# Performance work log

Measured on AMD Instinct MI355X. Metric: run time of the kernel, lower is better.

## Reference

```python
import jax, jax.numpy as jnp
import numpy as np

EPS = 1e-6
SKIP_THR = 0.35     # AdaptiveComputeBlock skip_threshold
ENERGY_THR = 0.95   # AdaptiveRankLinear energy_threshold


def rms_norm(x, w):
    return x * jax.lax.rsqrt(jnp.mean(x * x, axis=-1, keepdims=True) + EPS) * w


def ternary_quantize(w):
    # absmean quantization: round(w/scale) clamped to {-1,0,+1}, rescaled
    s = jnp.maximum(jnp.mean(jnp.abs(w)), 1e-8)
    return jnp.clip(jnp.round(w / s), -1.0, 1.0) * s


def setup_inputs() -> dict:
    key = jax.random.key(0)
    ks = jax.random.split(key, 16)
    D, H, depth, R, N = 2048, 8192, 2, 16, 4096
    inp = {
        "x": jax.random.normal(ks[0], (N, D), jnp.float32),
        "acb_norm_w": jnp.ones((depth, D), jnp.float32),
        "router_w": jax.random.normal(ks[1], (depth, D), jnp.float32) * 0.02,
        "w1": jax.random.normal(ks[2], (depth, H, D), jnp.float32) * 0.02,
        "w2": jax.random.normal(ks[3], (depth, D, H), jnp.float32) * 0.02,
        "w3": jax.random.normal(ks[4], (depth, H, D), jnp.float32) * 0.02,
        "acb_gamma": jax.random.uniform(ks[5], (depth, D), jnp.float32) * 1e-2,
        "arl_norm_w": jnp.ones((depth, D), jnp.float32),
        "U": jax.random.normal(ks[6], (depth, D, R), jnp.float32) * 0.02,
        "S": jax.random.normal(ks[7], (depth, R), jnp.float32),
        "V": jax.random.normal(ks[8], (depth, R, D), jnp.float32) * 0.02,
        "arl_gamma": jax.random.uniform(ks[9], (depth, D), jnp.float32) * 1e-2,
        "bit_norm_w": jnp.ones((depth, D), jnp.float32),
        "w_up": jax.random.normal(ks[10], (depth, H, D), jnp.float32) * 0.02,
        "w_down": jax.random.normal(ks[11], (depth, D, H), jnp.float32) * 0.02,
        "bit_gamma": jax.random.uniform(ks[12], (depth, D), jnp.float32) * 1e-2,
    }
    return inp


def reference(x, acb_norm_w, router_w, w1, w2, w3, acb_gamma,
              arl_norm_w, U, S, V, arl_gamma,
              bit_norm_w, w_up, w_down, bit_gamma):
    depth = acb_norm_w.shape[0]
    for d in range(depth):
        # ---- AdaptiveComputeBlock (eval path: hard router mask, no gate scaling)
        xn = rms_norm(x, acb_norm_w[d])                    # [N, D]
        gates = jax.nn.sigmoid(xn @ router_w[d])           # [N]
        active = (gates > SKIP_THR)[..., None]             # [N, 1]
        h = jax.nn.silu(xn @ w1[d].T) * (xn @ w3[d].T)     # [N, H] SwiGLU
        ffn = h @ w2[d].T                                  # [N, D]
        x = x + jnp.where(active, ffn * acb_gamma[d], 0.0)

        # ---- AdaptiveRankLinear (effective-rank mask from singular energy)
        xn = rms_norm(x, arl_norm_w[d])
        s_abs = jnp.abs(S[d])
        cum = jnp.cumsum(s_abs) / jnp.maximum(jnp.sum(s_abs), 1e-8)
        # index i kept iff i < r, r = first index with cum >= threshold (plus 1)
        keep = jnp.concatenate([jnp.ones((1,), bool), cum[:-1] < ENERGY_THR])
        low = (xn @ U[d]) * (S[d] * keep)                  # [N, R]
        x = x + (low @ V[d]) * arl_gamma[d]

        # ---- BitLinear (eval path: ternary weights, fp activations)
        xn = rms_norm(x, bit_norm_w[d])
        hq = jax.nn.silu(xn @ ternary_quantize(w_up[d]).T)  # [N, H]
        x = x + (hq @ ternary_quantize(w_down[d]).T) * bit_gamma[d]
    return x
```

## Files before the change

### kernel.cpp

```cpp
#include <hip/hip_runtime.h>

#define D_DIM 2048
#define H_DIM 8192
#define NTOK  4096
#define R_DIM 16
#define DEPTH 2

typedef float f32x4 __attribute__((ext_vector_type(4)));
typedef unsigned short u16x4 __attribute__((ext_vector_type(4)));
typedef unsigned short u16x8 __attribute__((ext_vector_type(8)));
typedef int i32x2 __attribute__((ext_vector_type(2)));
typedef int i32x4 __attribute__((ext_vector_type(4)));

typedef __attribute__((address_space(1))) void void_g;
typedef __attribute__((address_space(3))) void void_l;

__device__ __forceinline__ unsigned short f2bf(float f){
  __bf16 b = (__bf16)f;
  return __builtin_bit_cast(unsigned short, b);
}
__device__ __forceinline__ float bf2f(unsigned short u){
  unsigned int x = ((unsigned int)u) << 16;
  return __builtin_bit_cast(float, x);
}

__device__ __forceinline__ float wredf(float v){
#pragma unroll
  for(int o=32;o;o>>=1) v += __shfl_xor(v,o,64);
  return v;
}
__device__ __forceinline__ float wredmax(float v){
#pragma unroll
  for(int o=32;o;o>>=1) v = fmaxf(v, __shfl_xor(v,o,64));
  return v;
}
__device__ __forceinline__ double wredd(double v){
#pragma unroll
  for(int o=32;o;o>>=1) v += __shfl_xor(v,o,64);
  return v;
}

__device__ __forceinline__ void gload_lds16(const void* g, void* l){
  __builtin_amdgcn_global_load_lds((void_g*)g, (void_l*)l, 16, 0, 0);
}

__device__ __forceinline__ int clampi(int v, int lim){
  return v > lim ? lim : (v < -lim ? -lim : v);
}
__device__ __forceinline__ int pack4q(float a, float b, float c, float d,
                                      float inv, int lim){
  int qa = clampi((int)rintf(a*inv), lim);
  int qb = clampi((int)rintf(b*inv), lim);
  int qc = clampi((int)rintf(c*inv), lim);
  int qd = clampi((int)rintf(d*inv), lim);
  return (qa&255) | ((qb&255)<<8) | ((qc&255)<<16) | ((qd&255)<<24);
}

__global__ __launch_bounds__(256) void rowpass1_i8(
    const float* __restrict__ x, const float* __restrict__ nw,
    const float* __restrict__ rw, signed char* __restrict__ xq,
    float* __restrict__ sxn, float* __restrict__ act)
{
  const int row = blockIdx.x, tid = threadIdx.x;
  const int lane = tid & 63, wid = tid >> 6;
  const float* xr = x + (size_t)row*D_DIM + tid*8;
  f32x4 v0 = *(const f32x4*)xr;
  f32x4 v1 = *(const f32x4*)(xr+4);
  float ssq = 0.0f;
#pragma unroll
  for(int j=0;j<4;++j) ssq += v0[j]*v0[j] + v1[j]*v1[j];
  __shared__ float red[4];
  float t = wredf(ssq);
  if(lane==0) red[wid] = t;
  __syncthreads();
  const float rs = rsqrtf((red[0]+red[1]+red[2]+red[3])*(1.0f/D_DIM) + 1e-6f);

  f32x4 n0 = *(const f32x4*)(nw + tid*8);
  f32x4 n1 = *(const f32x4*)(nw + tid*8 + 4);
  f32x4 r0 = *(const f32x4*)(rw + tid*8);
  f32x4 r1 = *(const f32x4*)(rw + tid*8 + 4);
  float a[8];
  float gp = 0.0f, am = 0.0f;
#pragma unroll
  for(int j=0;j<4;++j){
    a[j]   = v0[j]*rs*n0[j];
    a[4+j] = v1[j]*rs*n1[j];
    gp += a[j]*r0[j] + a[4+j]*r1[j];
    am = fmaxf(am, fmaxf(fabsf(a[j]), fabsf(a[4+j])));
  }
  float wm = wredmax(am);
  __syncthreads();
  if(lane==0) red[wid] = wm;
  __syncthreads();
  const float rowmax = fmaxf(fmaxf(red[0],red[1]), fmaxf(red[2],red[3]));
  const float guard = fmaxf(rowmax, 1e-12f);
  const float inv = 127.0f/guard;
  i32x2 q;
  q[0] = pack4q(a[0],a[1],a[2],a[3], inv, 127);
  q[1] = pack4q(a[4],a[5],a[6],a[7], inv, 127);
  *(i32x2*)(xq + (size_t)row*D_DIM + tid*8) = q;

  float gd = wredf(gp);
  __syncthreads();
  if(lane==0) red[wid] = gd;
  __syncthreads();
  if(tid==0){
    sxn[row] = guard/127.0f;
    float dot = red[0]+red[1]+red[2]+red[3];
    float g = 1.0f/(1.0f+expf(-dot));
    act[row] = (g > 0.35f) ? 1.0f : 0.0f;
  }
}

__global__ __launch_bounds__(256) void buildmap(const float* __restrict__ act,
                                                int* __restrict__ rowmap,
                                                int* __restrict__ cntp)
{
  const int tid = threadIdx.x;
  const int lane = tid & 63, wid = tid >> 6;
  int flags[16]; int c = 0;
#pragma unroll
  for(int j=0;j<16;++j){
    flags[j] = (act[tid*16+j] != 0.0f) ? 1 : 0;
    c += flags[j];
  }
  int inc = c;
#pragma unroll
  for(int o=1;o<64;o<<=1){
    int t = __shfl_up(inc, o, 64);
    if(lane >= o) inc += t;
  }
  __shared__ int wsum[4];
  if(lane==63) wsum[wid] = inc;
  __syncthreads();
  int base = inc - c;
  for(int w=0;w<wid;++w) base += wsum[w];
  const int total = wsum[0]+wsum[1]+wsum[2]+wsum[3];
#pragma unroll
  for(int j=0;j<16;++j){
    if(flags[j]) rowmap[base++] = tid*16+j;
  }
  if(tid==0) cntp[0] = total;
  __syncthreads();
  for(int i = total + tid; i < NTOK; i += 256) rowmap[i] = 0;
}

__global__ __launch_bounds__(256) void rowpass2_i8(
    float* __restrict__ x, const float* __restrict__ anw,
    const float* __restrict__ U, const float* __restrict__ Sv,
    const float* __restrict__ V, const float* __restrict__ agam,
    const float* __restrict__ bnw, signed char* __restrict__ xq,
    float* __restrict__ sxn)
{
  const int row = blockIdx.x, tid = threadIdx.x;
  const int lane = tid & 63, wid = tid >> 6;
  float* xr = x + (size_t)row*D_DIM + tid*8;
  f32x4 v0 = *(const f32x4*)xr;
  f32x4 v1 = *(const f32x4*)(xr+4);
  float ssq = 0.0f;
#pragma unroll
  for(int j=0;j<4;++j) ssq += v0[j]*v0[j] + v1[j]*v1[j];
  __shared__ float red[4];
  float t = wredf(ssq);
  if(lane==0) red[wid] = t;
  __syncthreads();
  const float rs = rsqrtf((red[0]+red[1]+red[2]+red[3])*(1.0f/D_DIM) + 1e-6f);

  f32x4 a0 = *(const f32x4*)(anw + tid*8);
  f32x4 a1 = *(const f32x4*)(anw + tid*8 + 4);
  float xn2[8];
#pragma unroll
  for(int j=0;j<4;++j){ xn2[j] = v0[j]*rs*a0[j]; xn2[4+j] = v1[j]*rs*a1[j]; }

  float pl[16];
#pragma unroll
  for(int r2=0;r2<16;++r2) pl[r2] = 0.0f;
#pragma unroll
  for(int j=0;j<8;++j){
    const int k = tid*8 + j;
    const f32x4* Up = (const f32x4*)(U + (size_t)k*R_DIM);
    f32x4 u0=Up[0], u1=Up[1], u2=Up[2], u3=Up[3];
    const float xv = xn2[j];
#pragma unroll
    for(int q=0;q<4;++q){
      pl[q]    += xv*u0[q];
      pl[4+q]  += xv*u1[q];
      pl[8+q]  += xv*u2[q];
      pl[12+q] += xv*u3[q];
    }
  }
#pragma unroll
  for(int r2=0;r2<16;++r2) pl[r2] = wredf(pl[r2]);
  __shared__ float lred[4][16];
  if(lane==0){
#pragma unroll
    for(int r2=0;r2<16;++r2) lred[wid][r2] = pl[r2];
  }
  __syncthreads();
  __shared__ float lowS[16];
  if(tid==0){
    float sa[16]; float totS = 0.0f;
#pragma unroll
    for(int r2=0;r2<16;++r2){ sa[r2] = fabsf(Sv[r2]); totS += sa[r2]; }
    totS = fmaxf(totS, 1e-8f);
    float c = 0.0f;
#pragma unroll
    for(int r2=0;r2<16;++r2){
      float lraw = lred[0][r2]+lred[1][r2]+lred[2][r2]+lred[3][r2];
      float keep = (r2==0) ? 1.0f : ((c/totS < 0.95f) ? 1.0f : 0.0f);
      c += sa[r2];
      lowS[r2] = lraw * Sv[r2] * keep;
    }
  }
  __syncthreads();

  f32x4 d0 = {0,0,0,0}, d1 = {0,0,0,0};
#pragma unroll
  for(int r2=0;r2<16;++r2){
    const float lr = lowS[r2];
    const f32x4* Vp = (const f32x4*)(V + (size_t)r2*D_DIM + tid*8);
    f32x4 q0 = Vp[0], q1 = Vp[1];
#pragma unroll
    for(int j=0;j<4;++j){ d0[j] += lr*q0[j]; d1[j] += lr*q1[j]; }
  }
  f32x4 g0 = *(const f32x4*)(agam + tid*8);
  f32x4 g1 = *(const f32x4*)(agam + tid*8 + 4);
  f32x4 xo0, xo1;
  float ssq2 = 0.0f;
#pragma unroll
  for(int j=0;j<4;++j){
    xo0[j] = v0[j] + d0[j]*g0[j];
    xo1[j] = v1[j] + d1[j]*g1[j];
    ssq2 += xo0[j]*xo0[j] + xo1[j]*xo1[j];
  }
  __syncthreads();
  float t2 = wredf(ssq2);
  if(lane==0) red[wid] = t2;
  __syncthreads();
  const float rs2 = rsqrtf((red[0]+red[1]+red[2]+red[3])*(1.0f/D_DIM) + 1e-6f);
  f32x4 b0 = *(const f32x4*)(bnw + tid*8);
  f32x4 b1 = *(const f32x4*)(bnw + tid*8 + 4);
  float a[8]; float am = 0.0f;
#pragma unroll
  for(int j=0;j<4;++j){
    a[j]   = xo0[j]*rs2*b0[j];
    a[4+j] = xo1[j]*rs2*b1[j];
    am = fmaxf(am, fmaxf(fabsf(a[j]), fabsf(a[4+j])));
  }
  *(f32x4*)xr = xo0;
  *(f32x4*)(xr+4) = xo1;

  float wm = wredmax(am);
  __syncthreads();
  if(lane==0) red[wid] = wm;
  __syncthreads();
  const float rowmax = fmaxf(fmaxf(red[0],red[1]), fmaxf(red[2],red[3]));
  const float guard = fmaxf(rowmax, 1e-12f);
  const float inv = 127.0f/guard;
  i32x2 q;
  q[0] = pack4q(a[0],a[1],a[2],a[3], inv, 127);
  q[1] = pack4q(a[4],a[5],a[6],a[7], inv, 127);
  *(i32x2*)(xq + (size_t)row*D_DIM + tid*8) = q;
  if(tid==0) sxn[row] = guard/127.0f;
}

__global__ __launch_bounds__(256) void hquant(
    const unsigned short* __restrict__ h, signed char* __restrict__ q,
    float* __restrict__ sh, const int* __restrict__ cntp)
{
  const int row = blockIdx.x, tid = threadIdx.x;
  if(cntp && row >= cntp[0]) return;
  const int lane = tid & 63, wid = tid >> 6;
  const unsigned short* hr = h + (size_t)row*H_DIM + tid*32;
  float v[32]; float am = 0.0f;
#pragma unroll
  for(int c=0;c<4;++c){
    u16x8 u = *(const u16x8*)(hr + c*8);
#pragma unroll
    for(int j=0;j<8;++j){
      float f = bf2f(u[j]);
      v[c*8+j] = f;
      am = fmaxf(am, fabsf(f));
    }
  }
  __shared__ float red[4];
  float wm = wredmax(am);
  if(lane==0) red[wid] = wm;
  __syncthreads();
  const float rowmax = fmaxf(fmaxf(red[0],red[1]), fmaxf(red[2],red[3]));
  const float guard = fmaxf(rowmax, 1e-12f);
  const float inv = 127.0f/guard;
  i32x4 o0, o1;
#pragma unroll
  for(int c=0;c<4;++c)
    o0[c] = pack4q(v[c*4],v[c*4+1],v[c*4+2],v[c*4+3], inv, 127);
#pragma unroll
  for(int c=0;c<4;++c)
    o1[c] = pack4q(v[16+c*4],v[16+c*4+1],v[16+c*4+2],v[16+c*4+3], inv, 127);
  signed char* qp = q + (size_t)row*H_DIM + tid*32;
  *(i32x4*)qp = o0;
  *(i32x4*)(qp+16) = o1;
  if(tid==0) sh[row] = guard/127.0f;
}

template<int C>
__global__ __launch_bounds__(256) void wquant_row(const float* __restrict__ w,
                                                  signed char* __restrict__ q,
                                                  float* __restrict__ srow)
{
  constexpr int PER = C/256;
  const int row = blockIdx.x, tid = threadIdx.x;
  const int lane = tid & 63, wid = tid >> 6;
  const float* wr = w + (size_t)row*C + tid*PER;
  float v[PER];
  float am = 0.0f;
#pragma unroll
  for(int j=0;j<PER;j+=4){
    f32x4 t = *(const f32x4*)(wr+j);
#pragma unroll
    for(int e=0;e<4;++e){ v[j+e] = t[e]; am = fmaxf(am, fabsf(t[e])); }
  }
  float wm = wredmax(am);
  __shared__ float red[4];
  if(lane==0) red[wid] = wm;
  __syncthreads();
  const float guard = fmaxf(fmaxf(fmaxf(red[0],red[1]),fmaxf(red[2],red[3])),
                            1e-12f);
  const float inv = 127.0f/guard;
  signed char* qr = q + (size_t)row*C + tid*PER;
#pragma unroll
  for(int j=0;j<PER;j+=8){
    i32x2 o;
    o[0] = pack4q(v[j],v[j+1],v[j+2],v[j+3], inv, 127);
    o[1] = pack4q(v[j+4],v[j+5],v[j+6],v[j+7], inv, 127);
    *(i32x2*)(qr+j) = o;
  }
  if(tid==0) srow[row] = guard/127.0f;
}

__global__ __launch_bounds__(256) void wq2(
    const float* __restrict__ wa, const float* __restrict__ wb,
    signed char* __restrict__ qa, signed char* __restrict__ qb,
    float* __restrict__ sa, float* __restrict__ sb)
{
  const int bid = blockIdx.x, tid = threadIdx.x;
  const int lane = tid & 63, wid = tid >> 6;
  const int row = (bid < H_DIM) ? bid : bid - H_DIM;
  const float* src = ((bid < H_DIM) ? wa : wb) + (size_t)row*D_DIM + tid*8;
  signed char* dq  = ((bid < H_DIM) ? qa : qb) + (size_t)row*D_DIM + tid*8;
  float* sd        = ((bid < H_DIM) ? sa : sb) + row;
  f32x4 v0 = *(const f32x4*)src;
  f32x4 v1 = *(const f32x4*)(src+4);
  float am = 0.0f;
#pragma unroll
  for(int e=0;e<4;++e)
    am = fmaxf(am, fmaxf(fabsf(v0[e]), fabsf(v1[e])));
  float wm = wredmax(am);
  __shared__ float red[4];
  if(lane==0) red[wid] = wm;
  __syncthreads();
  const float guard = fmaxf(fmaxf(fmaxf(red[0],red[1]),fmaxf(red[2],red[3])),
                            1e-12f);
  const float inv = 127.0f/guard;
  i32x2 o;
  o[0] = pack4q(v0[0],v0[1],v0[2],v0[3], inv, 127);
  o[1] = pack4q(v1[0],v1[1],v1[2],v1[3], inv, 127);
  *(i32x2*)dq = o;
  if(tid==0) *sd = guard/127.0f;
}

__global__ __launch_bounds__(256) void abs_part2(const float* __restrict__ wa,
                                                 const float* __restrict__ wb,
                                                 double* __restrict__ part)
{
  const long long n4 = (long long)H_DIM*D_DIM/4;
  const int bid = blockIdx.x, tid = threadIdx.x;
  const int lane = tid & 63, wid = tid >> 6;
  const float* w = (bid < 1024) ? wa : wb;
  const int sub = bid & 1023;
  float s = 0.0f;
  for(long long i = (long long)sub*256 + tid; i < n4; i += 1024*256){
    f32x4 v = ((const f32x4*)w)[i];
    s += fabsf(v[0]) + fabsf(v[1]) + fabsf(v[2]) + fabsf(v[3]);
  }
  double ds = wredd((double)s);
  __shared__ double sred[4];
  if(lane==0) sred[wid] = ds;
  __syncthreads();
  if(tid==0) part[bid] = sred[0]+sred[1]+sred[2]+sred[3];
}

__global__ __launch_bounds__(256) void abs_final2(const double* __restrict__ part,
                                                  float* __restrict__ scale)
{
  const int tid = threadIdx.x;
  const int lane = tid & 63, wid = tid >> 6;
  double s0 = 0.0, s1 = 0.0;
  for(int i=tid;i<1024;i+=256){ s0 += part[i]; s1 += part[1024+i]; }
  s0 = wredd(s0); s1 = wredd(s1);
  __shared__ double sred[2][4];
  if(lane==0){ sred[0][wid] = s0; sred[1][wid] = s1; }
  __syncthreads();
  if(tid==0){
    double m0 = (sred[0][0]+sred[0][1]+sred[0][2]+sred[0][3])
                / ((double)H_DIM*(double)D_DIM);
    double m1 = (sred[1][0]+sred[1][1]+sred[1][2]+sred[1][3])
                / ((double)H_DIM*(double)D_DIM);
    scale[0] = (float)fmax(m0, 1e-8);
    scale[1] = (float)fmax(m1, 1e-8);
  }
}

__global__ __launch_bounds__(256) void tquant2(const float* __restrict__ wa,
                                               const float* __restrict__ wb,
                                               const float* __restrict__ scale,
                                               signed char* __restrict__ qa,
                                               signed char* __restrict__ qb)
{
  const long long n8 = (long long)H_DIM*D_DIM/8;
  const int bid = blockIdx.x;
  const bool first = (bid < 2048);
  const float* w = first ? wa : wb;
  signed char* q = first ? qa : qb;
  const float inv = 1.0f/scale[first ? 0 : 1];
  const int sub = first ? bid : bid - 2048;
  for(long long i = (long long)sub*256 + threadIdx.x; i < n8; i += 2048*256){
    f32x4 a = ((const f32x4*)w)[2*i];
    f32x4 b = ((const f32x4*)w)[2*i+1];
    i32x2 o;
    o[0] = pack4q(a[0],a[1],a[2],a[3], inv, 1);
    o[1] = pack4q(b[0],b[1],b[2],b[3], inv, 1);
    ((i32x2*)q)[i] = o;
  }
}

template<int EPI>
__global__ __launch_bounds__(256, 2) void gemmq(
    const signed char* __restrict__ A,
    const signed char* __restrict__ B0,
    const signed char* __restrict__ B1,
    const int Nout, const int K,
    const float* __restrict__ sArow,
    const float* __restrict__ sW0,
    const float* __restrict__ sW1,
    const int* __restrict__ rowmap,
    const int* __restrict__ cntp,
    unsigned short* __restrict__ obf,
    float* __restrict__ xacc,
    const float* __restrict__ gamma)
{
  constexpr bool DUAL    = (EPI==0);
  constexpr bool GATHER  = (EPI==0);
  constexpr bool SCATTER = (EPI==2);
  constexpr bool CMP     = GATHER || SCATTER;

  __shared__ __align__(16) signed char smA[128*128];
  __shared__ __align__(16) signed char smB[128*128];
  __shared__ __align__(16) signed char smB2[DUAL?(128*128):16];

  int cnt = 0;
  if constexpr (CMP) cnt = cntp[0];
  const int padded = CMP ? ((cnt+127)&~127) : (1<<30);

  const int tid  = threadIdx.x;
  const int lane = tid & 63;
  const int wid  = tid >> 6;
  const int wr   = wid >> 1;
  const int wc   = wid & 1;
  const int frow = lane & 15;
  const int k16  = lane >> 4;

  const int nwg = (int)gridDim.x;
  const int bid = (int)blockIdx.x;
  const int swz = ((bid & 7) * (nwg >> 3)) + (bid >> 3);
  const int rowBase = (swz & 31) << 7;
  const int colBase = (swz >> 5) << 7;

  if constexpr (CMP){ if(rowBase >= padded) return; }

  const signed char* Asrc[4];
  const signed char* Bsrc[4];
  const signed char* B2src[4];
#pragma unroll
  for(int u=0;u<4;++u){
    int L = u*256 + tid;
    int row = L >> 3, c = L & 7;
    int soff = (c ^ (row & 7)) * 16;
    int arow;
    if constexpr (GATHER) arow = rowmap[rowBase + row];
    else                  arow = rowBase + row;
    Asrc[u] = A + (size_t)arow*K + soff;
    Bsrc[u] = B0 + (size_t)(colBase + row)*K + soff;
    if constexpr (DUAL) B2src[u] = B1 + (size_t)(colBase + row)*K + soff;
  }

  const i32x4 izero = {0,0,0,0};
  i32x4 acc[4][4];
  i32x4 acc2[4][4];
#pragma unroll
  for(int m=0;m<4;++m)
#pragma unroll
    for(int n=0;n<4;++n){ acc[m][n] = izero; acc2[m][n] = izero; }

  for(int k0=0;k0<K;k0+=128){
#pragma unroll
    for(int u=0;u<4;++u) gload_lds16(Asrc[u]+k0, &smA[u*4096 + tid*16]);
#pragma unroll
    for(int u=0;u<4;++u) gload_lds16(Bsrc[u]+k0, &smB[u*4096 + tid*16]);
    if constexpr (DUAL){
#pragma unroll
      for(int u=0;u<4;++u) gload_lds16(B2src[u]+k0, &smB2[u*4096 + tid*16]);
    }
    __syncthreads();

#pragma unroll
    for(int ks=0;ks<2;++ks){
      i32x4 af[4], bfr[4], bfr2[4];
#pragma unroll
      for(int m=0;m<4;++m){
        int rr = (wr<<6)+(m<<4)+frow;
        int cc = (ks*4 + k16) ^ (rr & 7);
        af[m] = *(const i32x4*)&smA[rr*128 + cc*16];
      }
#pragma unroll
      for(int n=0;n<4;++n){
        int rr = (wc<<6)+(n<<4)+frow;
        int cc = (ks*4 + k16) ^ (rr & 7);
        bfr[n] = *(const i32x4*)&smB[rr*128 + cc*16];
        if constexpr (DUAL) bfr2[n] = *(const i32x4*)&smB2[rr*128 + cc*16];
      }
#pragma unroll
      for(int m=0;m<4;++m)
#pragma unroll
        for(int n=0;n<4;++n){
          acc[m][n] = __builtin_amdgcn_mfma_i32_16x16x64_i8(af[m], bfr[n], acc[m][n], 0,0,0);
          if constexpr (DUAL)
            acc2[m][n] = __builtin_amdgcn_mfma_i32_16x16x64_i8(af[m], bfr2[n], acc2[m][n], 0,0,0);
        }
    }
    __syncthreads();
  }

  float fsW0 = 0.0f;
  if constexpr (EPI==1 || EPI==3) fsW0 = sW0[0];
  const int growB = rowBase + (wr<<6) + (k16<<2);
  const int gcolB = colBase + (wc<<6) + frow;
#pragma unroll
  for(int m=0;m<4;++m){
#pragma unroll
    for(int n=0;n<4;++n){
      const int grow0 = growB + (m<<4);
      const int gcol  = gcolB + (n<<4);
      i32x4 v = acc[m][n];
      if constexpr (EPI==0){
        i32x4 v2 = acc2[m][n];
        const float w0 = sW0[gcol];
        const float w1s = sW1[gcol];
#pragma unroll
        for(int j=0;j<4;++j){
          const int mc = grow0 + j;
          const float sa = sArow[rowmap[mc]];
          float f1 = (float)v[j]  * sa * w0;
          float f3 = (float)v2[j] * sa * w1s;
          float hv = (f1/(1.0f+__expf(-f1))) * f3;
          obf[(size_t)mc*Nout + gcol] = f2bf(hv);
        }
      } else if constexpr (EPI==1){
#pragma unroll
        for(int j=0;j<4;++j){
          const int mc = grow0 + j;
          const float sa = sArow[mc];
          float f = (float)v[j] * sa * fsW0;
          obf[(size_t)mc*Nout + gcol] = f2bf(f/(1.0f+__expf(-f)));
        }
      } else if constexpr (EPI==2){
        const float gw = sW0[gcol]*gamma[gcol];
#pragma unroll
        for(int j=0;j<4;++j){
          const int mc = grow0 + j;
          if(mc < cnt){
            const float sa = sArow[mc];
            xacc[(size_t)rowmap[mc]*Nout + gcol] += (float)v[j] * sa * gw;
          }
        }
      } else {
        const float gw = fsW0*gamma[gcol];
#pragma unroll
        for(int j=0;j<4;++j){
          const int mc = grow0 + j;
          const float sa = sArow[mc];
          xacc[(size_t)mc*Nout + gcol] += (float)v[j] * sa * gw;
        }
      }
    }
  }
}

extern "C" void kernel_launch(void* const* d_in, const int* in_sizes, int n_in,
                              void* d_out, int out_size, void* d_ws, size_t ws_size,
                              hipStream_t stream)
{
  (void)in_sizes; (void)n_in; (void)out_size; (void)ws_size;
  const float* x_in  = (const float*)d_in[0];
  const float* acbnw = (const float*)d_in[1];
  const float* routw = (const float*)d_in[2];
  const float* w1    = (const float*)d_in[3];
  const float* w2    = (const float*)d_in[4];
  const float* w3    = (const float*)d_in[5];
  const float* acbg  = (const float*)d_in[6];
  const float* arlnw = (const float*)d_in[7];
  const float* U     = (const float*)d_in[8];
  const float* Sv    = (const float*)d_in[9];
  const float* V     = (const float*)d_in[10];
  const float* arlg  = (const float*)d_in[11];
  const float* bitnw = (const float*)d_in[12];
  const float* wup   = (const float*)d_in[13];
  const float* wdn   = (const float*)d_in[14];
  const float* bitg  = (const float*)d_in[15];

  float* xs = (float*)d_out;
  char* ws = (char*)d_ws;

  hipMemcpyAsync(xs, x_in, (size_t)NTOK*D_DIM*sizeof(float),
                 hipMemcpyDeviceToDevice, stream);

  const size_t MB = 1048576;
  unsigned short* hb   = (unsigned short*)(ws);
  signed char*    xnq  = (signed char*)(ws + 64*MB);
  signed char*    hbq  = (signed char*)(ws + 72*MB);
  signed char*    slotA= (signed char*)(ws + 104*MB);
  signed char*    slotB= (signed char*)(ws + 120*MB);
  signed char*    slotC= (signed char*)(ws + 136*MB);
  char* tail = ws + 152*MB;
  float*  sxn   = (float*)(tail);
  float*  sh    = (float*)(tail + 16384);
  float*  act   = (float*)(tail + 32768);
  double* dpart = (double*)(tail + 49152);
  float*  scb   = (float*)(tail + 65536);
  float*  sWA   = (float*)(tail + 69632);
  float*  sWB   = (float*)(tail + 102400);
  int*    rowmap= (int*)(tail + 135168);
  int*    cntp  = (int*)(tail + 151552);

  const int gH = 2048;
  const int gD = 512;

  for(int d=0; d<DEPTH; ++d){
    const size_t oD  = (size_t)d*D_DIM;
    const size_t oHD = (size_t)d*H_DIM*D_DIM;
    const size_t oR  = (size_t)d*R_DIM;
    const size_t oDR = (size_t)d*D_DIM*R_DIM;

    wq2<<<2*H_DIM,256,0,stream>>>(w1+oHD, w3+oHD, slotA, slotB, sWA, sWB);
    rowpass1_i8<<<NTOK,256,0,stream>>>(xs, acbnw+oD, routw+oD, xnq, sxn, act);
    buildmap<<<1,256,0,stream>>>(act, rowmap, cntp);
    gemmq<0><<<gH,256,0,stream>>>(
        xnq, slotA, slotB, H_DIM, D_DIM, sxn, sWA, sWB, rowmap, cntp,
        hb, nullptr, nullptr);
    hquant<<<NTOK,256,0,stream>>>(hb, hbq, sh, cntp);
    wquant_row<H_DIM><<<D_DIM,256,0,stream>>>(w2+oHD, slotA, sWA);
    gemmq<2><<<gD,256,0,stream>>>(
        hbq, slotA, nullptr, D_DIM, H_DIM, sh, sWA, nullptr, rowmap, cntp,
        nullptr, xs, acbg+oD);

    rowpass2_i8<<<NTOK,256,0,stream>>>(xs, arlnw+oD, U+oDR, Sv+oR, V+oDR,
                                       arlg+oD, bitnw+oD, xnq, sxn);

    abs_part2<<<2048,256,0,stream>>>(wup+oHD, wdn+oHD, dpart);
    abs_final2<<<1,256,0,stream>>>(dpart, scb);
    tquant2<<<4096,256,0,stream>>>(wup+oHD, wdn+oHD, scb, slotB, slotC);
    gemmq<1><<<gH,256,0,stream>>>(
        xnq, slotB, nullptr, H_DIM, D_DIM, sxn, scb+0, nullptr,
        nullptr, nullptr, hb, nullptr, nullptr);
    hquant<<<NTOK,256,0,stream>>>(hb, hbq, sh, nullptr);
    gemmq<3><<<gD,256,0,stream>>>(
        hbq, slotC, nullptr, D_DIM, H_DIM, sh, scb+1, nullptr,
        nullptr, nullptr, nullptr, xs, bitg+oD);
  }
}
```

Measured before the change: 1.413 ms.

## Merge small kernels into combined launches and fold input copy into rowpass

Several small kernels are merged into larger multi-role launches that branch on block index: buildmap goes into the w1/w3 quantization kernel, hquant is combined with the w2 row quantization, and the abs-sum partial reduction is combined with the second rowpass. The initial device-to-device copy of x is removed, and the first rowpass writes x to the output buffer as it reads it. The aim is fewer kernel launches and launch gaps, plus independent work running concurrently in one grid. The cost is more branchy kernels whose blocks have uneven work, and a larger shared-memory and register footprint per kernel.

```diff
diff --git a/kernel.cpp b/kernel.cpp
--- a/kernel.cpp
+++ b/kernel.cpp
@@ -57,15 +57,21 @@
 }
 
 __global__ __launch_bounds__(256) void rowpass1_i8(
-    const float* __restrict__ x, const float* __restrict__ nw,
-    const float* __restrict__ rw, signed char* __restrict__ xq,
-    float* __restrict__ sxn, float* __restrict__ act)
+    const float* __restrict__ xsrc, float* __restrict__ xcopy,
+    const float* __restrict__ nw, const float* __restrict__ rw,
+    signed char* __restrict__ xq, float* __restrict__ sxn,
+    float* __restrict__ act)
 {
   const int row = blockIdx.x, tid = threadIdx.x;
   const int lane = tid & 63, wid = tid >> 6;
-  const float* xr = x + (size_t)row*D_DIM + tid*8;
+  const float* xr = xsrc + (size_t)row*D_DIM + tid*8;
   f32x4 v0 = *(const f32x4*)xr;
   f32x4 v1 = *(const f32x4*)(xr+4);
+  if(xcopy){
+    float* xc = xcopy + (size_t)row*D_DIM + tid*8;
+    *(f32x4*)xc = v0;
+    *(f32x4*)(xc+4) = v1;
+  }
   float ssq = 0.0f;
 #pragma unroll
   for(int j=0;j<4;++j) ssq += v0[j]*v0[j] + v1[j]*v1[j];
@@ -112,48 +118,100 @@
   }
 }
 
-__global__ __launch_bounds__(256) void buildmap(const float* __restrict__ act,
-                                                int* __restrict__ rowmap,
-                                                int* __restrict__ cntp)
-{
-  const int tid = threadIdx.x;
+__global__ __launch_bounds__(256) void wq2b(
+    const float* __restrict__ wa, const float* __restrict__ wb,
+    signed char* __restrict__ qa, signed char* __restrict__ qb,
+    float* __restrict__ sa, float* __restrict__ sb,
+    const float* __restrict__ act, int* __restrict__ rowmap,
+    int* __restrict__ cntp)
+{
+  const int bid = blockIdx.x, tid = threadIdx.x;
   const int lane = tid & 63, wid = tid >> 6;
-  int flags[16]; int c = 0;
-#pragma unroll
-  for(int j=0;j<16;++j){
-    flags[j] = (act[tid*16+j] != 0.0f) ? 1 : 0;
-    c += flags[j];
-  }
-  int inc = c;
-#pragma unroll
-  for(int o=1;o<64;o<<=1){
-    int t = __shfl_up(inc, o, 64);
-    if(lane >= o) inc += t;
-  }
-  __shared__ int wsum[4];
-  if(lane==63) wsum[wid] = inc;
-  __syncthreads();
-  int base = inc - c;
-  for(int w=0;w<wid;++w) base += wsum[w];
-  const int total = wsum[0]+wsum[1]+wsum[2]+wsum[3];
-#pragma unroll
-  for(int j=0;j<16;++j){
-    if(flags[j]) rowmap[base++] = tid*16+j;
-  }
-  if(tid==0) cntp[0] = total;
-  __syncthreads();
-  for(int i = total + tid; i < NTOK; i += 256) rowmap[i] = 0;
-}
-
-__global__ __launch_bounds__(256) void rowpass2_i8(
+
+  if(bid == 2*H_DIM){
+    int flags[16]; int c = 0;
+#pragma unroll
+    for(int j=0;j<16;++j){
+      flags[j] = (act[tid*16+j] != 0.0f) ? 1 : 0;
+      c += flags[j];
+    }
+    int inc = c;
+#pragma unroll
+    for(int o=1;o<64;o<<=1){
+      int t = __shfl_up(inc, o, 64);
+      if(lane >= o) inc += t;
+    }
+    __shared__ int wsum[4];
+    if(lane==63) wsum[wid] = inc;
+    __syncthreads();
+    int base = inc - c;
+    for(int w=0;w<wid;++w) base += wsum[w];
+    const int total = wsum[0]+wsum[1]+wsum[2]+wsum[3];
+#pragma unroll
+    for(int j=0;j<16;++j){
+      if(flags[j]) rowmap[base++] = tid*16+j;
+    }
+    if(tid==0) cntp[0] = total;
+    __syncthreads();
+    for(int i = total + tid; i < NTOK; i += 256) rowmap[i] = 0;
+    return;
+  }
+
+  const int row = (bid < H_DIM) ? bid : bid - H_DIM;
+  const float* src = ((bid < H_DIM) ? wa : wb) + (size_t)row*D_DIM + tid*8;
+  signed char* dq  = ((bid < H_DIM) ? qa : qb) + (size_t)row*D_DIM + tid*8;
+  float* sd        = ((bid < H_DIM) ? sa : sb) + row;
+  f32x4 v0 = *(const f32x4*)src;
+  f32x4 v1 = *(const f32x4*)(src+4);
+  float am = 0.0f;
+#pragma unroll
+  for(int e=0;e<4;++e)
+    am = fmaxf(am, fmaxf(fabsf(v0[e]), fabsf(v1[e])));
+  float wm = wredmax(am);
+  __shared__ float red[4];
+  if(lane==0) red[wid] = wm;
+  __syncthreads();
+  const float guard = fmaxf(fmaxf(fmaxf(red[0],red[1]),fmaxf(red[2],red[3])),
+                            1e-12f);
+  const float inv = 127.0f/guard;
+  i32x2 o;
+  o[0] = pack4q(v0[0],v0[1],v0[2],v0[3], inv, 127);
+  o[1] = pack4q(v1[0],v1[1],v1[2],v1[3], inv, 127);
+  *(i32x2*)dq = o;
+  if(tid==0) *sd = guard/127.0f;
+}
+
+__global__ __launch_bounds__(256) void rp2_abs(
     float* __restrict__ x, const float* __restrict__ anw,
     const float* __restrict__ U, const float* __restrict__ Sv,
     const float* __restrict__ V, const float* __restrict__ agam,
     const float* __restrict__ bnw, signed char* __restrict__ xq,
-    float* __restrict__ sxn)
-{
-  const int row = blockIdx.x, tid = threadIdx.x;
+    float* __restrict__ sxn,
+    const float* __restrict__ wa, const float* __restrict__ wb,
+    double* __restrict__ part)
+{
+  const int bid = blockIdx.x, tid = threadIdx.x;
   const int lane = tid & 63, wid = tid >> 6;
+
+  if(bid >= NTOK){
+    const long long n4 = (long long)H_DIM*D_DIM/4;
+    const int b2 = bid - NTOK;
+    const float* w = (b2 < 1024) ? wa : wb;
+    const int sub = b2 & 1023;
+    float s = 0.0f;
+    for(long long i = (long long)sub*256 + tid; i < n4; i += 1024*256){
+      f32x4 v = ((const f32x4*)w)[i];
+      s += fabsf(v[0]) + fabsf(v[1]) + fabsf(v[2]) + fabsf(v[3]);
+    }
+    double ds = wredd((double)s);
+    __shared__ double sred[4];
+    if(lane==0) sred[wid] = ds;
+    __syncthreads();
+    if(tid==0) part[b2] = sred[0]+sred[1]+sred[2]+sred[3];
+    return;
+  }
+
+  const int row = bid;
   float* xr = x + (size_t)row*D_DIM + tid*8;
   f32x4 v0 = *(const f32x4*)xr;
   f32x4 v1 = *(const f32x4*)(xr+4);
@@ -303,91 +361,77 @@
   if(tid==0) sh[row] = guard/127.0f;
 }
 
-template<int C>
-__global__ __launch_bounds__(256) void wquant_row(const float* __restrict__ w,
-                                                  signed char* __restrict__ q,
-                                                  float* __restrict__ srow)
-{
-  constexpr int PER = C/256;
-  const int row = blockIdx.x, tid = threadIdx.x;
-  const int lane = tid & 63, wid = tid >> 6;
-  const float* wr = w + (size_t)row*C + tid*PER;
-  float v[PER];
-  float am = 0.0f;
-#pragma unroll
-  for(int j=0;j<PER;j+=4){
-    f32x4 t = *(const f32x4*)(wr+j);
-#pragma unroll
-    for(int e=0;e<4;++e){ v[j+e] = t[e]; am = fmaxf(am, fabsf(t[e])); }
-  }
-  float wm = wredmax(am);
-  __shared__ float red[4];
-  if(lane==0) red[wid] = wm;
-  __syncthreads();
-  const float guard = fmaxf(fmaxf(fmaxf(red[0],red[1]),fmaxf(red[2],red[3])),
-                            1e-12f);
-  const float inv = 127.0f/guard;
-  signed char* qr = q + (size_t)row*C + tid*PER;
-#pragma unroll
-  for(int j=0;j<PER;j+=8){
-    i32x2 o;
-    o[0] = pack4q(v[j],v[j+1],v[j+2],v[j+3], inv, 127);
-    o[1] = pack4q(v[j+4],v[j+5],v[j+6],v[j+7], inv, 127);
-    *(i32x2*)(qr+j) = o;
-  }
-  if(tid==0) srow[row] = guard/127.0f;
-}
-
-__global__ __launch_bounds__(256) void wq2(
-    const float* __restrict__ wa, const float* __restrict__ wb,
-    signed char* __restrict__ qa, signed char* __restrict__ qb,
-    float* __restrict__ sa, float* __restrict__ sb)
+__global__ __launch_bounds__(256) void hq_wq(
+    const unsigned short* __restrict__ h, signed char* __restrict__ q,
+    float* __restrict__ sh, const int* __restrict__ cntp,
+    const float* __restrict__ w2, signed char* __restrict__ qw,
+    float* __restrict__ sw)
 {
   const int bid = blockIdx.x, tid = threadIdx.x;
   const int lane = tid & 63, wid = tid >> 6;
-  const int row = (bid < H_DIM) ? bid : bid - H_DIM;
-  const float* src = ((bid < H_DIM) ? wa : wb) + (size_t)row*D_DIM + tid*8;
-  signed char* dq  = ((bid < H_DIM) ? qa : qb) + (size_t)row*D_DIM + tid*8;
-  float* sd        = ((bid < H_DIM) ? sa : sb) + row;
-  f32x4 v0 = *(const f32x4*)src;
-  f32x4 v1 = *(const f32x4*)(src+4);
-  float am = 0.0f;
-#pragma unroll
-  for(int e=0;e<4;++e)
-    am = fmaxf(am, fmaxf(fabsf(v0[e]), fabsf(v1[e])));
+
+  if(bid >= NTOK){
+    const int row = bid - NTOK;
+    const float* wr = w2 + (size_t)row*H_DIM + tid*32;
+    float v[32];
+    float am = 0.0f;
+#pragma unroll
+    for(int j=0;j<32;j+=4){
+      f32x4 t = *(const f32x4*)(wr+j);
+#pragma unroll
+      for(int e=0;e<4;++e){ v[j+e] = t[e]; am = fmaxf(am, fabsf(t[e])); }
+    }
+    float wm = wredmax(am);
+    __shared__ float redw[4];
+    if(lane==0) redw[wid] = wm;
+    __syncthreads();
+    const float guard = fmaxf(fmaxf(fmaxf(redw[0],redw[1]),
+                                    fmaxf(redw[2],redw[3])), 1e-12f);
+    const float inv = 127.0f/guard;
+    signed char* qr = qw + (size_t)row*H_DIM + tid*32;
+#pragma unroll
+    for(int j=0;j<32;j+=8){
+      i32x2 o;
+      o[0] = pack4q(v[j],v[j+1],v[j+2],v[j+3], inv, 127);
+      o[1] = pack4q(v[j+4],v[j+5],v[j+6],v[j+7], inv, 127);
+      *(i32x2*)(qr+j) = o;
+    }
+    if(tid==0) sw[row] = guard/127.0f;
+    return;
+  }
+
+  const int row = bid;
+  if(row >= cntp[0]) return;
+  const unsigned short* hr = h + (size_t)row*H_DIM + tid*32;
+  float v[32]; float am = 0.0f;
+#pragma unroll
+  for(int c=0;c<4;++c){
+    u16x8 u = *(const u16x8*)(hr + c*8);
+#pragma unroll
+    for(int j=0;j<8;++j){
+      float f = bf2f(u[j]);
+      v[c*8+j] = f;
+      am = fmaxf(am, fabsf(f));
+    }
+  }
+  __shared__ float red[4];
   float wm = wredmax(am);
-  __shared__ float red[4];
   if(lane==0) red[wid] = wm;
   __syncthreads();
-  const float guard = fmaxf(fmaxf(fmaxf(red[0],red[1]),fmaxf(red[2],red[3])),
-                            1e-12f);
+  const float rowmax = fmaxf(fmaxf(red[0],red[1]), fmaxf(red[2],red[3]));
+  const float guard = fmaxf(rowmax, 1e-12f);
   const float inv = 127.0f/guard;
-  i32x2 o;
-  o[0] = pack4q(v0[0],v0[1],v0[2],v0[3], inv, 127);
-  o[1] = pack4q(v1[0],v1[1],v1[2],v1[3], inv, 127);
-  *(i32x2*)dq = o;
-  if(tid==0) *sd = guard/127.0f;
-}
-
-__global__ __launch_bounds__(256) void abs_part2(const float* __restrict__ wa,
-                                                 const float* __restrict__ wb,
-                                                 double* __restrict__ part)
-{
-  const long long n4 = (long long)H_DIM*D_DIM/4;
-  const int bid = blockIdx.x, tid = threadIdx.x;
-  const int lane = tid & 63, wid = tid >> 6;
-  const float* w = (bid < 1024) ? wa : wb;
-  const int sub = bid & 1023;
-  float s = 0.0f;
-  for(long long i = (long long)sub*256 + tid; i < n4; i += 1024*256){
-    f32x4 v = ((const f32x4*)w)[i];
-    s += fabsf(v[0]) + fabsf(v[1]) + fabsf(v[2]) + fabsf(v[3]);
-  }
-  double ds = wredd((double)s);
-  __shared__ double sred[4];
-  if(lane==0) sred[wid] = ds;
-  __syncthreads();
-  if(tid==0) part[bid] = sred[0]+sred[1]+sred[2]+sred[3];
+  i32x4 o0, o1;
+#pragma unroll
+  for(int c=0;c<4;++c)
+    o0[c] = pack4q(v[c*4],v[c*4+1],v[c*4+2],v[c*4+3], inv, 127);
+#pragma unroll
+  for(int c=0;c<4;++c)
+    o1[c] = pack4q(v[16+c*4],v[16+c*4+1],v[16+c*4+2],v[16+c*4+3], inv, 127);
+  signed char* qp = q + (size_t)row*H_DIM + tid*32;
+  *(i32x4*)qp = o0;
+  *(i32x4*)(qp+16) = o1;
+  if(tid==0) sh[row] = guard/127.0f;
 }
 
 __global__ __launch_bounds__(256) void abs_final2(const double* __restrict__ part,
@@ -621,9 +665,6 @@
   float* xs = (float*)d_out;
   char* ws = (char*)d_ws;
 
-  hipMemcpyAsync(xs, x_in, (size_t)NTOK*D_DIM*sizeof(float),
-                 hipMemcpyDeviceToDevice, stream);
-
   const size_t MB = 1048576;
   unsigned short* hb   = (unsigned short*)(ws);
   signed char*    xnq  = (signed char*)(ws + 64*MB);
@@ -651,22 +692,24 @@
     const size_t oR  = (size_t)d*R_DIM;
     const size_t oDR = (size_t)d*D_DIM*R_DIM;
 
-    wq2<<<2*H_DIM,256,0,stream>>>(w1+oHD, w3+oHD, slotA, slotB, sWA, sWB);
-    rowpass1_i8<<<NTOK,256,0,stream>>>(xs, acbnw+oD, routw+oD, xnq, sxn, act);
-    buildmap<<<1,256,0,stream>>>(act, rowmap, cntp);
+    rowpass1_i8<<<NTOK,256,0,stream>>>(
+        (d==0) ? x_in : xs, (d==0) ? xs : nullptr,
+        acbnw+oD, routw+oD, xnq, sxn, act);
+    wq2b<<<2*H_DIM+1,256,0,stream>>>(w1+oHD, w3+oHD, slotA, slotB, sWA, sWB,
+                                     act, rowmap, cntp);
     gemmq<0><<<gH,256,0,stream>>>(
         xnq, slotA, slotB, H_DIM, D_DIM, sxn, sWA, sWB, rowmap, cntp,
         hb, nullptr, nullptr);
-    hquant<<<NTOK,256,0,stream>>>(hb, hbq, sh, cntp);
-    wquant_row<H_DIM><<<D_DIM,256,0,stream>>>(w2+oHD, slotA, sWA);
+    hq_wq<<<NTOK+D_DIM,256,0,stream>>>(hb, hbq, sh, cntp,
+                                       w2+oHD, slotA, sWA);
     gemmq<2><<<gD,256,0,stream>>>(
         hbq, slotA, nullptr, D_DIM, H_DIM, sh, sWA, nullptr, rowmap, cntp,
         nullptr, xs, acbg+oD);
 
-    rowpass2_i8<<<NTOK,256,0,stream>>>(xs, arlnw+oD, U+oDR, Sv+oR, V+oDR,
-                                       arlg+oD, bitnw+oD, xnq, sxn);
-
-    abs_part2<<<2048,256,0,stream>>>(wup+oHD, wdn+oHD, dpart);
+    rp2_abs<<<NTOK+2048,256,0,stream>>>(xs, arlnw+oD, U+oDR, Sv+oR, V+oDR,
+                                        arlg+oD, bitnw+oD, xnq, sxn,
+                                        wup+oHD, wdn+oHD, dpart);
+
     abs_final2<<<1,256,0,stream>>>(dpart, scb);
     tquant2<<<4096,256,0,stream>>>(wup+oHD, wdn+oHD, scb, slotB, slotC);
     gemmq<1><<<gH,256,0,stream>>>(
```

Result: no change. 1.441 ms (+2.0%).
